# Kernel optimization log

Hardware: AMD Instinct MI355X
Metric: run time of the kernel (lower is better)

The kernel has to match this reference:

```python
import math
import jax, jax.numpy as jnp
import numpy as np

B, C, H, W = 8, 128, 128, 128

def _cosine_basis(n):
    pos = (jnp.arange(n, dtype=jnp.float32) + 0.5) / n          # [n]
    freq = jnp.arange(n, dtype=jnp.float32)[:, None]            # [n,1]
    basis = jnp.cos(freq * pos[None, :] * math.pi) * math.sqrt(2.0 / n)
    return basis.at[0, :].multiply(1.0 / math.sqrt(2.0))        # [n,n]


def setup_inputs() -> dict:
    key = jax.random.key(0)
    ks = jax.random.split(key, 12)
    s = 0.02
    return {
        "x":        jax.random.normal(ks[0], (B, C, H, W), jnp.float32),
        "dw_w":     jax.random.normal(ks[1], (C, 1, 3, 3), jnp.float32) * s,
        "dw_b":     jnp.zeros((C,), jnp.float32),
        "in_w":     jax.random.normal(ks[2], (2 * C, C), jnp.float32) * s,
        "in_b":     jnp.zeros((2 * C,), jnp.float32),
        "out_w":    jax.random.normal(ks[3], (C, C), jnp.float32) * s,
        "out_b":    jnp.zeros((C,), jnp.float32),
        "ln_w":     jnp.ones((C,), jnp.float32),
        "ln_b":     jnp.zeros((C,), jnp.float32),
        "ph_w":     jax.random.normal(ks[4], (C, C), jnp.float32) * s,
        "ph_b":     jnp.zeros((C,), jnp.float32),
        "wave_speed": jnp.ones((1,), jnp.float32),
        "damping":    jnp.full((1,), 0.1, jnp.float32),
        "freq_embed": jax.random.normal(ks[5], (H, W, C), jnp.float32) * s,
    }


def reference(x, dw_w, dw_b, in_w, in_b, out_w, out_b, ln_w, ln_b,
              ph_w, ph_b, wave_speed, damping, freq_embed):
    # depthwise 3x3 conv (groups=C), padding=1
    mixed = jax.lax.conv_general_dilated(
        x, dw_w, window_strides=(1, 1), padding=((1, 1), (1, 1)),
        dimension_numbers=("NCHW", "OIHW", "NCHW"), feature_group_count=C)
    mixed = mixed + dw_b[None, :, None, None]
    mixed = jnp.transpose(mixed, (0, 2, 3, 1))                  # [B,H,W,C]

    proj = mixed @ in_w.T + in_b                                # [B,H,W,2C]
    carrier, gate = jnp.split(proj, 2, axis=-1)

    cos_h = _cosine_basis(H)
    cos_w = _cosine_basis(W)
    # DCT-II along H then W
    spectral = jnp.einsum("bhwc,nh->bnwc", carrier, cos_h)
    spectral = jnp.einsum("bnwc,mw->bnmc", spectral, cos_w)     # [B,H,W,C] (freq)

    # phase modulation (base_resolution == H == W, so no resize)
    phase = jax.nn.gelu(freq_embed @ ph_w.T + ph_b, approximate=False)  # [H,W,C]
    wave_phase = wave_speed * phase                             # broadcast [H,W,C]
    vel_scale = jnp.sin(wave_phase) / jnp.maximum(jnp.abs(wave_speed), 1e-6)
    modulated = (jnp.cos(wave_phase) + vel_scale * (1.0 + 0.5 * damping)) * spectral

    # inverse DCT
    fused = jnp.einsum("bnmc,wm->bnwc", modulated, cos_w.T)
    fused = jnp.einsum("bnwc,hn->bhwc", fused, cos_h.T)         # [B,H,W,C]

    # LayerNorm over channels
    mu = jnp.mean(fused, axis=-1, keepdims=True)
    var = jnp.mean(jnp.square(fused - mu), axis=-1, keepdims=True)
    fused = (fused - mu) / jnp.sqrt(var + 1e-5) * ln_w + ln_b

    fused = fused * jax.nn.silu(gate)
    out = fused @ out_w.T + out_b                               # [B,H,W,C]
    return jnp.transpose(out, (0, 3, 1, 2))                     # [B,C,H,W]
```

## Files before the change

kernel.cpp:

```cpp
#include <hip/hip_runtime.h>
#include <math.h>

#ifndef M_PI
#define M_PI 3.14159265358979323846
#endif

typedef float fx4 __attribute__((ext_vector_type(4)));
typedef __bf16 bf16x8 __attribute__((ext_vector_type(8)));
typedef __bf16 bf16x4 __attribute__((ext_vector_type(4)));

__device__ __forceinline__ unsigned short f2bf(float f){
  union { float f; unsigned u; } v; v.f = f;
  unsigned r = v.u + 0x7FFFu + ((v.u >> 16) & 1u);
  return (unsigned short)(r >> 16);
}
__device__ __forceinline__ float bf2f(unsigned short u){
  union { unsigned u; float f; } v; v.u = ((unsigned)u) << 16;
  return v.f;
}
__device__ __forceinline__ int swz(int row, int colbyte){
  return row*256 + (colbyte ^ ((row & 7) << 4));
}

template<typename FA, typename FB>
__device__ __forceinline__ void run_gemm(FA la, FB lb, fx4 (&acc)[4][4]){
  bf16x8 a[2][4], b[2][4];
  #pragma unroll
  for (int mi=0;mi<4;mi++){ a[0][mi]=la(mi,0); b[0][mi]=lb(mi,0); }
  #pragma unroll
  for (int ks=0; ks<4; ks++){
    int cur = ks&1, nxt = cur^1;
    if (ks<3){
      #pragma unroll
      for (int mi=0;mi<4;mi++){ a[nxt][mi]=la(mi,ks+1); b[nxt][mi]=lb(mi,ks+1); }
    }
    #pragma unroll
    for (int mi=0;mi<4;mi++)
      #pragma unroll
      for (int ni=0;ni<4;ni++)
        acc[mi][ni] = __builtin_amdgcn_mfma_f32_16x16x32_bf16(a[cur][mi], b[cur][ni], acc[mi][ni], 0, 0, 0);
  }
}

template<typename FA0, typename FA1, typename FB>
__device__ __forceinline__ void run_pair_sharedB(FA0 la0, FA1 la1, FB lb,
                                                 fx4 (&acc0)[4][4], fx4 (&acc1)[4][4]){
  bf16x8 a0[2][4], a1[2][4], b[2][4];
  #pragma unroll
  for (int mi=0;mi<4;mi++){ a0[0][mi]=la0(mi,0); a1[0][mi]=la1(mi,0); b[0][mi]=lb(mi,0); }
  #pragma unroll
  for (int ks=0; ks<4; ks++){
    int cur = ks&1, nxt = cur^1;
    if (ks<3){
      #pragma unroll
      for (int mi=0;mi<4;mi++){ a0[nxt][mi]=la0(mi,ks+1); a1[nxt][mi]=la1(mi,ks+1); b[nxt][mi]=lb(mi,ks+1); }
    }
    #pragma unroll
    for (int mi=0;mi<4;mi++)
      #pragma unroll
      for (int ni=0;ni<4;ni++){
        acc0[mi][ni] = __builtin_amdgcn_mfma_f32_16x16x32_bf16(a0[cur][mi], b[cur][ni], acc0[mi][ni], 0, 0, 0);
        acc1[mi][ni] = __builtin_amdgcn_mfma_f32_16x16x32_bf16(a1[cur][mi], b[cur][ni], acc1[mi][ni], 0, 0, 0);
      }
  }
}

template<typename FA, typename FB0, typename FB1>
__device__ __forceinline__ void run_pair_sharedA(FA la, FB0 lb0, FB1 lb1,
                                                 fx4 (&acc0)[4][4], fx4 (&acc1)[4][4]){
  bf16x8 a[2][4], b0[2][4], b1[2][4];
  #pragma unroll
  for (int mi=0;mi<4;mi++){ a[0][mi]=la(mi,0); b0[0][mi]=lb0(mi,0); b1[0][mi]=lb1(mi,0); }
  #pragma unroll
  for (int ks=0; ks<4; ks++){
    int cur = ks&1, nxt = cur^1;
    if (ks<3){
      #pragma unroll
      for (int mi=0;mi<4;mi++){ a[nxt][mi]=la(mi,ks+1); b0[nxt][mi]=lb0(mi,ks+1); b1[nxt][mi]=lb1(mi,ks+1); }
    }
    #pragma unroll
    for (int mi=0;mi<4;mi++)
      #pragma unroll
      for (int ni=0;ni<4;ni++){
        acc0[mi][ni] = __builtin_amdgcn_mfma_f32_16x16x32_bf16(a[cur][mi], b0[cur][ni], acc0[mi][ni], 0, 0, 0);
        acc1[mi][ni] = __builtin_amdgcn_mfma_f32_16x16x32_bf16(a[cur][mi], b1[cur][ni], acc1[mi][ni], 0, 0, 0);
      }
  }
}

__global__ __launch_bounds__(128) void prep_kernel(
    const float* __restrict__ in_w, const float* __restrict__ ph_w,
    const float* __restrict__ out_w,
    unsigned short* __restrict__ basis_bf, unsigned short* __restrict__ basisT_bf,
    unsigned short* __restrict__ ph_w_bf, unsigned short* __restrict__ in_w_bf,
    unsigned short* __restrict__ out_w_bf)
{
  int n = blockIdx.x;
  int h = threadIdx.x;
  double arg = (double)(n*(2*h+1)) * (M_PI/256.0);
  double v = cos(arg) * 0.125;
  if (n==0) v *= 0.7071067811865476;
  unsigned short bv = f2bf((float)v);
  basis_bf[n*128+h]  = bv;
  basisT_bf[h*128+n] = bv;
  ph_w_bf[n*128+h]  = f2bf(ph_w[n*128+h]);
  in_w_bf[n*128+h]        = f2bf(in_w[n*128+h]);
  in_w_bf[(n+128)*128+h]  = f2bf(in_w[(n+128)*128+h]);
  out_w_bf[n*128+h]       = f2bf(out_w[n*128+h]);
}

__global__ __launch_bounds__(256) void castfe_kernel(
  const float* __restrict__ fe, unsigned short* __restrict__ feb)
{
  int idx = blockIdx.x*256 + threadIdx.x;
  const float* s = fe + (size_t)idx*8;
  float4 f0 = *(const float4*)s;
  float4 f1 = *(const float4*)(s+4);
  unsigned short o[8];
  o[0]=f2bf(f0.x); o[1]=f2bf(f0.y); o[2]=f2bf(f0.z); o[3]=f2bf(f0.w);
  o[4]=f2bf(f1.x); o[5]=f2bf(f1.y); o[6]=f2bf(f1.z); o[7]=f2bf(f1.w);
  *(int4*)(feb + (size_t)idx*8) = *(const int4*)o;
}

__global__ __launch_bounds__(256) void projk_kernel(
  const unsigned short* __restrict__ feb, const unsigned short* __restrict__ ph_w_bf,
  float* __restrict__ projT)
{
  int r0 = blockIdx.x * 128;
  int t = threadIdx.x;
  int l = t & 63, wid = t >> 6;
  int wm = wid >> 1, wn = wid & 1;
  int lr = l & 15, lk = (l>>4)*8, ld4 = (l>>4)*4;
  fx4 acc[4][4];
  #pragma unroll
  for (int i=0;i<4;i++) for (int j=0;j<4;j++) acc[i][j] = (fx4){0.f,0.f,0.f,0.f};
  run_gemm(
    [&](int mi,int ks)->bf16x8{ return *(const bf16x8*)(feb + (size_t)(r0 + wm*64+mi*16+lr)*128 + ks*32+lk); },
    [&](int ni,int ks)->bf16x8{ return *(const bf16x8*)(ph_w_bf + (size_t)(wn*64+ni*16+lr)*128 + ks*32+lk); },
    acc);
  #pragma unroll
  for (int mi=0;mi<4;mi++)
    #pragma unroll
    for (int ni=0;ni<4;ni++){
      int c = wn*64 + ni*16 + lr;
      int r = r0 + wm*64 + mi*16 + ld4;
      *(fx4*)(projT + (size_t)c*16384 + r) = acc[mi][ni];
    }
}

__global__ __launch_bounds__(256) void modfin_kernel(
  const float* __restrict__ projT, const float* __restrict__ ph_b,
  const float* __restrict__ wave_speed, const float* __restrict__ damping,
  float* __restrict__ modT)
{
  int blk = blockIdx.x;
  int c = blk >> 4, qb = blk & 15;
  int t = threadIdx.x;
  int q = qb*8 + (t>>5);
  int p0 = (t & 31)*4;
  float ws0 = wave_speed[0];
  float dmp = damping[0];
  float inv = 1.0f / fmaxf(fabsf(ws0), 1e-6f);
  float dampf = 1.0f + 0.5f*dmp;
  float bc = ph_b[c];
  const float* src = projT + (size_t)c*16384 + q;
  float o[4];
  #pragma unroll
  for (int i=0;i<4;i++){
    float v = src[(size_t)(p0+i)*128] + bc;
    float g = 0.5f*v*(1.0f + erff(v*0.70710678118f));
    float wp = ws0*g;
    o[i] = __cosf(wp) + __sinf(wp)*inv*dampf;
  }
  *(float4*)(modT + ((size_t)c*128 + q)*128 + p0) = make_float4(o[0],o[1],o[2],o[3]);
}

__global__ __launch_bounds__(256) void dwconv_kernel(
  const float* __restrict__ x, const float* __restrict__ dw_w,
  const float* __restrict__ dw_b, unsigned short* __restrict__ conv)
{
  int blk = blockIdx.x;
  int plane = blk >> 2, band = blk & 3;
  int c = plane & 127;
  const float* xp = x + (size_t)plane*16384;
  unsigned short* op = conv + (size_t)plane*16384;
  const float* kw = dw_w + c*9;
  float k0=kw[0],k1=kw[1],k2=kw[2],k3=kw[3],k4=kw[4],k5=kw[5],k6=kw[6],k7=kw[7],k8=kw[8];
  float bias = dw_b[c];
  int t = threadIdx.x;
  int q = t & 31;
  int w0 = q*4;
  int rg = t >> 5;
  int h0 = band*32 + rg*4;
  bool le = (q==0), re = (q==31);

  float4 fA, fB, fC; float lA,rA,lB,rB,lC,rC;
  #define LOADROW(hh, f, l, r) { \
    int hc = (hh)<0 ? 0 : ((hh)>127 ? 127 : (hh)); \
    f = *(const float4*)(xp + hc*128 + w0); \
    float lu = __shfl_up(f.w, 1, 32); \
    float rd = __shfl_down(f.x, 1, 32); \
    l = le ? 0.f : lu; \
    r = re ? 0.f : rd; \
    if ((hh)<0 || (hh)>127){ f = make_float4(0.f,0.f,0.f,0.f); l=0.f; r=0.f; } \
  }
  LOADROW(h0-1, fA,lA,rA);
  LOADROW(h0,   fB,lB,rB);
  #pragma unroll
  for (int i=0;i<4;i++){
    LOADROW(h0+1+i, fC,lC,rC);
    float4 o;
    o.x = bias; o.y = bias; o.z = bias; o.w = bias;
    o.x = fmaf(k0,lA,  fmaf(k1,fA.x, fmaf(k2,fA.y, o.x)));
    o.y = fmaf(k0,fA.x,fmaf(k1,fA.y, fmaf(k2,fA.z, o.y)));
    o.z = fmaf(k0,fA.y,fmaf(k1,fA.z, fmaf(k2,fA.w, o.z)));
    o.w = fmaf(k0,fA.z,fmaf(k1,fA.w, fmaf(k2,rA,   o.w)));
    o.x = fmaf(k3,lB,  fmaf(k4,fB.x, fmaf(k5,fB.y, o.x)));
    o.y = fmaf(k3,fB.x,fmaf(k4,fB.y, fmaf(k5,fB.z, o.y)));
    o.z = fmaf(k3,fB.y,fmaf(k4,fB.z, fmaf(k5,fB.w, o.z)));
    o.w = fmaf(k3,fB.z,fmaf(k4,fB.w, fmaf(k5,rB,   o.w)));
    o.x = fmaf(k6,lC,  fmaf(k7,fC.x, fmaf(k8,fC.y, o.x)));
    o.y = fmaf(k6,fC.x,fmaf(k7,fC.y, fmaf(k8,fC.z, o.y)));
    o.z = fmaf(k6,fC.y,fmaf(k7,fC.z, fmaf(k8,fC.w, o.z)));
    o.w = fmaf(k6,fC.z,fmaf(k7,fC.w, fmaf(k8,rC,   o.w)));
    bf16x4 v;
    v[0]=(__bf16)o.x; v[1]=(__bf16)o.y; v[2]=(__bf16)o.z; v[3]=(__bf16)o.w;
    *(bf16x4*)(op + (size_t)(h0+i)*128 + w0) = v;
    fA=fB; lA=lB; rA=rB;
    fB=fC; lB=lC; rB=rC;
  }
  #undef LOADROW
}

__global__ __launch_bounds__(512) void inproj_kernel(
  const unsigned short* __restrict__ conv, const unsigned short* __restrict__ in_w_bf,
  const float* __restrict__ in_b, unsigned short* __restrict__ carrier,
  unsigned short* __restrict__ gate)
{
  __shared__ char A[32768];
  int blk = blockIdx.x; int b = blk>>7, h = blk&127;
  const unsigned short* C = conv + (size_t)b*2097152 + h*128;
  int t = threadIdx.x;
  {
    int wl = t & 63, grp = t >> 6;
    #pragma unroll
    for (int p=0;p<2;p++){
      int w = wl + 64*p;
      #pragma unroll
      for (int q=0;q<4;q++){
        int c0 = (q*8 + grp)*4;
        ushort4 v;
        v.x = C[(size_t)(c0+0)*16384 + w];
        v.y = C[(size_t)(c0+1)*16384 + w];
        v.z = C[(size_t)(c0+2)*16384 + w];
        v.w = C[(size_t)(c0+3)*16384 + w];
        *(ushort4*)(A + swz(w, c0*2)) = v;
      }
    }
  }
  __syncthreads();
  int l = t & 63, wid = t >> 6;
  int wm = wid >> 2, wn = wid & 3;
  int lr = l & 15, lk = (l>>4)*8, ld4 = (l>>4)*4;
  fx4 acc[4][4];
  #pragma unroll
  for (int i=0;i<4;i++) for (int j=0;j<4;j++) acc[i][j] = (fx4){0.f,0.f,0.f,0.f};
  run_gemm(
    [&](int mi,int ks)->bf16x8{ return *(const bf16x8*)(A + swz(wm*64+mi*16+lr, (ks*32+lk)*2)); },
    [&](int ni,int ks)->bf16x8{ return *(const bf16x8*)(in_w_bf + (size_t)(wn*64+ni*16+lr)*128 + ks*32+lk); },
    acc);
  __syncthreads();
  if (wn < 2){
    #pragma unroll
    for (int mi=0;mi<4;mi++)
      #pragma unroll
      for (int ni=0;ni<4;ni++){
        int n = wn*64 + ni*16 + lr;
        int w0 = wm*64 + mi*16 + ld4;
        float bias = in_b[n];
        ushort4 v;
        v.x=f2bf(acc[mi][ni][0]+bias); v.y=f2bf(acc[mi][ni][1]+bias);
        v.z=f2bf(acc[mi][ni][2]+bias); v.w=f2bf(acc[mi][ni][3]+bias);
        *(ushort4*)(carrier + (size_t)(b*128+n)*16384 + h*128 + w0) = v;
      }
  } else {
    #pragma unroll
    for (int mi=0;mi<4;mi++)
      #pragma unroll
      for (int ni=0;ni<4;ni++){
        int n = wn*64 + ni*16 + lr;
        int c = n - 128;
        int w0 = wm*64 + mi*16 + ld4;
        float bias = in_b[n];
        #pragma unroll
        for (int r=0;r<4;r++){
          float v = acc[mi][ni][r] + bias;
          float s = v / (1.0f + __expf(-v));
          *(unsigned short*)(A + swz(w0+r, c*2)) = f2bf(s);
        }
      }
  }
  __syncthreads();
  {
    unsigned short* gout = gate + (size_t)blk*16384;
    int w = t >> 2, cq = (t & 3) * 32;
    #pragma unroll
    for (int i=0;i<4;i++){
      int c0 = cq + i*8;
      int4 v = *(const int4*)(A + swz(w, c0*2));
      *(int4*)(gout + w*128 + c0) = v;
    }
  }
}

__global__ __launch_bounds__(256) void wave_kernel(
  const unsigned short* __restrict__ carrier,
  const unsigned short* __restrict__ basis,
  const unsigned short* __restrict__ basisT,
  const float* __restrict__ modT,
  unsigned short* __restrict__ fused)
{
  __shared__ char U0[32768];
  __shared__ char U1[32768];
  int blk = blockIdx.x;
  int c = blk & 127;
  const unsigned short* X0 = carrier + (size_t)blk*16384;
  const unsigned short* X1 = carrier + (size_t)(blk+512)*16384;
  unsigned short* F0 = fused + (size_t)blk*16384;
  unsigned short* F1 = fused + (size_t)(blk+512)*16384;
  int t = threadIdx.x;
  int l = t & 63, wid = t >> 6;
  int wm = wid >> 1, wn = wid & 1;
  int lr = l & 15, lk = (l>>4)*8, ld4 = (l>>4)*4;
  fx4 acc0[4][4], acc1[4][4];

  #define ZACC { _Pragma("unroll") for (int i=0;i<4;i++) _Pragma("unroll") for (int j=0;j<4;j++){ acc0[i][j]=(fx4){0.f,0.f,0.f,0.f}; acc1[i][j]=(fx4){0.f,0.f,0.f,0.f}; } }
  #define TSTORE(BUF0, BUF1, ROW, COL) { \
    _Pragma("unroll") for (int mi=0;mi<4;mi++) \
      _Pragma("unroll") for (int ni=0;ni<4;ni++){ \
        int rr = wn*64 + ni*16 + lr, cc = wm*64 + mi*16 + ld4; (void)rr; (void)cc; \
        bf16x4 v0, v1; \
        v0[0]=(__bf16)acc0[mi][ni][0]; v0[1]=(__bf16)acc0[mi][ni][1]; \
        v0[2]=(__bf16)acc0[mi][ni][2]; v0[3]=(__bf16)acc0[mi][ni][3]; \
        v1[0]=(__bf16)acc1[mi][ni][0]; v1[1]=(__bf16)acc1[mi][ni][1]; \
        v1[2]=(__bf16)acc1[mi][ni][2]; v1[3]=(__bf16)acc1[mi][ni][3]; \
        *(bf16x4*)(BUF0 + swz(rr, cc*2)) = v0; \
        *(bf16x4*)(BUF1 + swz(rr, cc*2)) = v1; \
      } }

  ZACC;
  run_pair_sharedB(
    [&](int mi,int ks)->bf16x8{ return *(const bf16x8*)(X0 + (size_t)(wm*64+mi*16+lr)*128 + ks*32+lk); },
    [&](int mi,int ks)->bf16x8{ return *(const bf16x8*)(X1 + (size_t)(wm*64+mi*16+lr)*128 + ks*32+lk); },
    [&](int ni,int ks)->bf16x8{ return *(const bf16x8*)(basis + (size_t)(wn*64+ni*16+lr)*128 + ks*32+lk); },
    acc0, acc1);
  TSTORE(U0, U1, m, h);
  __syncthreads();

  ZACC;
  run_pair_sharedA(
    [&](int mi,int ks)->bf16x8{ return *(const bf16x8*)(basis + (size_t)(wm*64+mi*16+lr)*128 + ks*32+lk); },
    [&](int ni,int ks)->bf16x8{ return *(const bf16x8*)(U0 + swz(wn*64+ni*16+lr, (ks*32+lk)*2)); },
    [&](int ni,int ks)->bf16x8{ return *(const bf16x8*)(U1 + swz(wn*64+ni*16+lr, (ks*32+lk)*2)); },
    acc0, acc1);
  {
    const float* Mc = modT + (size_t)c*16384;
    #pragma unroll
    for (int mi=0;mi<4;mi++)
      #pragma unroll
      for (int ni=0;ni<4;ni++){
        int n0 = wm*64 + mi*16 + ld4, m = wn*64 + ni*16 + lr;
        fx4 mv = *(const fx4*)(Mc + (size_t)m*128 + n0);
        acc0[mi][ni] *= mv;
        acc1[mi][ni] *= mv;
      }
  }
  __syncthreads();
  TSTORE(U0, U1, m, n);
  __syncthreads();

  ZACC;
  run_pair_sharedB(
    [&](int mi,int ks)->bf16x8{ return *(const bf16x8*)(U0 + swz(wm*64+mi*16+lr, (ks*32+lk)*2)); },
    [&](int mi,int ks)->bf16x8{ return *(const bf16x8*)(U1 + swz(wm*64+mi*16+lr, (ks*32+lk)*2)); },
    [&](int ni,int ks)->bf16x8{ return *(const bf16x8*)(basisT + (size_t)(wn*64+ni*16+lr)*128 + ks*32+lk); },
    acc0, acc1);
  __syncthreads();
  TSTORE(U0, U1, h, m);
  __syncthreads();

  ZACC;
  run_pair_sharedA(
    [&](int mi,int ks)->bf16x8{ return *(const bf16x8*)(basisT + (size_t)(wm*64+mi*16+lr)*128 + ks*32+lk); },
    [&](int ni,int ks)->bf16x8{ return *(const bf16x8*)(U0 + swz(wn*64+ni*16+lr, (ks*32+lk)*2)); },
    [&](int ni,int ks)->bf16x8{ return *(const bf16x8*)(U1 + swz(wn*64+ni*16+lr, (ks*32+lk)*2)); },
    acc0, acc1);
  #pragma unroll
  for (int mi=0;mi<4;mi++)
    #pragma unroll
    for (int ni=0;ni<4;ni++){
      int hh = wn*64 + ni*16 + lr, w0 = wm*64 + mi*16 + ld4;
      bf16x4 v0, v1;
      v0[0]=(__bf16)acc0[mi][ni][0]; v0[1]=(__bf16)acc0[mi][ni][1];
      v0[2]=(__bf16)acc0[mi][ni][2]; v0[3]=(__bf16)acc0[mi][ni][3];
      v1[0]=(__bf16)acc1[mi][ni][0]; v1[1]=(__bf16)acc1[mi][ni][1];
      v1[2]=(__bf16)acc1[mi][ni][2]; v1[3]=(__bf16)acc1[mi][ni][3];
      *(bf16x4*)(F0 + hh*128 + w0) = v0;
      *(bf16x4*)(F1 + hh*128 + w0) = v1;
    }
  #undef ZACC
  #undef TSTORE
}

__global__ __launch_bounds__(256) void final_kernel(
  const unsigned short* __restrict__ fused, const unsigned short* __restrict__ gate,
  const unsigned short* __restrict__ out_w_bf, const float* __restrict__ out_b,
  const float* __restrict__ ln_w, const float* __restrict__ ln_b,
  float* __restrict__ out)
{
  __shared__ char Fl[32768];
  __shared__ char Al[32768];
  __shared__ float red[256], red2[256];
  __shared__ float mu[128], rs[128];
  int blk = blockIdx.x; int b = blk>>7, h = blk&127;
  const unsigned short* Fsrc = fused + (size_t)b*2097152 + h*128;
  const unsigned short* G = gate + (size_t)blk*16384;
  int t = threadIdx.x;
  {
    int c = t>>1, wq = (t&1)*64;
    #pragma unroll
    for (int i=0;i<8;i++){
      int w0 = wq + i*8;
      int4 v = *(const int4*)(Fsrc + (size_t)c*16384 + w0);
      *(int4*)(Fl + swz(c, w0*2)) = v;
    }
  }
  __syncthreads();
  {
    int w = t&127, half = t>>7;
    float s=0.f, q=0.f;
    for (int i=0;i<64;i++){
      int c = half*64 + i;
      float f = bf2f(*(const unsigned short*)(Fl + swz(c, w*2)));
      s += f; q = fmaf(f,f,q);
    }
    red[t]=s; red2[t]=q;
  }
  __syncthreads();
  if (t < 128){
    float ss = red[t]+red[t+128], qq = red2[t]+red2[t+128];
    float m = ss*(1.f/128.f);
    float var = qq*(1.f/128.f) - m*m;
    mu[t]=m; rs[t]=rsqrtf(var+1e-5f);
  }
  __syncthreads();
  {
    int w = t>>1, cq = (t&1)*64;
    float m_ = mu[w], r_ = rs[w];
    #pragma unroll
    for (int i=0;i<8;i++){
      int c0 = cq + i*8;
      ushort4 g0 = *(const ushort4*)(G + (size_t)w*128 + c0);
      ushort4 g1 = *(const ushort4*)(G + (size_t)w*128 + c0 + 4);
      unsigned short ov[8];
      unsigned short gv[8] = {g0.x,g0.y,g0.z,g0.w,g1.x,g1.y,g1.z,g1.w};
      #pragma unroll
      for (int j=0;j<8;j++){
        int cc = c0+j;
        float f = bf2f(*(const unsigned short*)(Fl + swz(cc, w*2)));
        float a = fmaf((f-m_)*r_, ln_w[cc], ln_b[cc]) * bf2f(gv[j]);
        ov[j] = f2bf(a);
      }
      *(int4*)(Al + swz(w, c0*2)) = *(const int4*)ov;
    }
  }
  __syncthreads();
  int l = t & 63, wid = t >> 6;
  int wm = wid >> 1, wn = wid & 1;
  int lr = l & 15, lk = (l>>4)*8, ld4 = (l>>4)*4;
  fx4 acc[4][4];
  #pragma unroll
  for (int i=0;i<4;i++) for (int j=0;j<4;j++) acc[i][j] = (fx4){0.f,0.f,0.f,0.f};
  run_gemm(
    [&](int mi,int ks)->bf16x8{ return *(const bf16x8*)(Al + swz(wm*64+mi*16+lr, (ks*32+lk)*2)); },
    [&](int ni,int ks)->bf16x8{ return *(const bf16x8*)(out_w_bf + (size_t)(wn*64+ni*16+lr)*128 + ks*32+lk); },
    acc);
  #pragma unroll
  for (int mi=0;mi<4;mi++)
    #pragma unroll
    for (int ni=0;ni<4;ni++){
      int j = wn*64 + ni*16 + lr, w0 = wm*64 + mi*16 + ld4;
      float bj = out_b[j];
      fx4 o = acc[mi][ni];
      o[0]+=bj; o[1]+=bj; o[2]+=bj; o[3]+=bj;
      *(fx4*)(out + ((size_t)(b*128 + j)*128 + h)*128 + w0) = o;
    }
}

extern "C" void kernel_launch(void* const* d_in, const int* in_sizes, int n_in,
                              void* d_out, int out_size, void* d_ws, size_t ws_size,
                              hipStream_t stream)
{
  const float* x      = (const float*)d_in[0];
  const float* dw_w   = (const float*)d_in[1];
  const float* dw_b   = (const float*)d_in[2];
  const float* in_w   = (const float*)d_in[3];
  const float* in_b   = (const float*)d_in[4];
  const float* out_w  = (const float*)d_in[5];
  const float* out_b  = (const float*)d_in[6];
  const float* ln_w   = (const float*)d_in[7];
  const float* ln_b   = (const float*)d_in[8];
  const float* ph_w   = (const float*)d_in[9];
  const float* ph_b   = (const float*)d_in[10];
  const float* wsp    = (const float*)d_in[11];
  const float* dmp    = (const float*)d_in[12];
  const float* fe     = (const float*)d_in[13];
  float* outp = (float*)d_out;

  float* modT  = (float*)d_ws;
  float* projT = modT + 2097152;
  unsigned short* feb      = (unsigned short*)(projT + 2097152);
  unsigned short* conv     = feb     + 2097152;
  unsigned short* carrier  = conv    + 16777216;
  unsigned short* gate     = carrier + 16777216;
  unsigned short* fusedb   = gate    + 16777216;
  unsigned short* basis_bf = fusedb  + 16777216;
  unsigned short* basisT_bf= basis_bf + 16384;
  unsigned short* in_w_bf  = basisT_bf + 16384;
  unsigned short* out_w_bf = in_w_bf + 32768;
  unsigned short* ph_w_bf  = out_w_bf + 16384;

  prep_kernel<<<128,128,0,stream>>>(in_w, ph_w, out_w, basis_bf, basisT_bf, ph_w_bf, in_w_bf, out_w_bf);
  castfe_kernel<<<1024,256,0,stream>>>(fe, feb);
  projk_kernel<<<128,256,0,stream>>>(feb, ph_w_bf, projT);
  modfin_kernel<<<2048,256,0,stream>>>(projT, ph_b, wsp, dmp, modT);
  dwconv_kernel<<<4096,256,0,stream>>>(x, dw_w, dw_b, conv);
  inproj_kernel<<<1024,512,0,stream>>>(conv, in_w_bf, in_b, carrier, gate);
  wave_kernel<<<512,256,0,stream>>>(carrier, basis_bf, basisT_bf, modT, fusedb);
  final_kernel<<<1024,256,0,stream>>>(fusedb, gate, out_w_bf, out_b, ln_w, ln_b, outp);
}
```

Measured before the change: 171.9 us.

## Merge independent prep kernels and process two rows per in-projection block

Prep, feature-embedding cast and depthwise conv now run in one launch, with the block index choosing the role. The ph_w projection GEMM shares a launch with the input projection. The input projection now handles two H rows per block with a paired MFMA routine that reuses each in_w fragment for both rows. This cuts the kernel count from eight to six and halves in_w loads per row. In exchange it uses 64KB of LDS per block, which lowers occupancy, and projk blocks launched at 512 threads leave half their threads idle.

```diff
diff --git a/kernel.cpp b/kernel.cpp
--- a/kernel.cpp
+++ b/kernel.cpp
@@ -88,64 +88,222 @@
   }
 }
 
-__global__ __launch_bounds__(128) void prep_kernel(
+__global__ __launch_bounds__(256) void k1_prep_cast_conv(
     const float* __restrict__ in_w, const float* __restrict__ ph_w,
-    const float* __restrict__ out_w,
+    const float* __restrict__ out_w, const float* __restrict__ fe,
+    const float* __restrict__ x, const float* __restrict__ dw_w,
+    const float* __restrict__ dw_b,
     unsigned short* __restrict__ basis_bf, unsigned short* __restrict__ basisT_bf,
     unsigned short* __restrict__ ph_w_bf, unsigned short* __restrict__ in_w_bf,
-    unsigned short* __restrict__ out_w_bf)
+    unsigned short* __restrict__ out_w_bf, unsigned short* __restrict__ feb,
+    unsigned short* __restrict__ conv)
 {
-  int n = blockIdx.x;
-  int h = threadIdx.x;
-  double arg = (double)(n*(2*h+1)) * (M_PI/256.0);
-  double v = cos(arg) * 0.125;
-  if (n==0) v *= 0.7071067811865476;
-  unsigned short bv = f2bf((float)v);
-  basis_bf[n*128+h]  = bv;
-  basisT_bf[h*128+n] = bv;
-  ph_w_bf[n*128+h]  = f2bf(ph_w[n*128+h]);
-  in_w_bf[n*128+h]        = f2bf(in_w[n*128+h]);
-  in_w_bf[(n+128)*128+h]  = f2bf(in_w[(n+128)*128+h]);
-  out_w_bf[n*128+h]       = f2bf(out_w[n*128+h]);
-}
-
-__global__ __launch_bounds__(256) void castfe_kernel(
-  const float* __restrict__ fe, unsigned short* __restrict__ feb)
-{
-  int idx = blockIdx.x*256 + threadIdx.x;
-  const float* s = fe + (size_t)idx*8;
-  float4 f0 = *(const float4*)s;
-  float4 f1 = *(const float4*)(s+4);
-  unsigned short o[8];
-  o[0]=f2bf(f0.x); o[1]=f2bf(f0.y); o[2]=f2bf(f0.z); o[3]=f2bf(f0.w);
-  o[4]=f2bf(f1.x); o[5]=f2bf(f1.y); o[6]=f2bf(f1.z); o[7]=f2bf(f1.w);
-  *(int4*)(feb + (size_t)idx*8) = *(const int4*)o;
-}
-
-__global__ __launch_bounds__(256) void projk_kernel(
+  int blk = blockIdx.x;
+  int t = threadIdx.x;
+  if (blk < 128){
+    if (t >= 128) return;
+    int n = blk, h = t;
+    double arg = (double)(n*(2*h+1)) * (M_PI/256.0);
+    double v = cos(arg) * 0.125;
+    if (n==0) v *= 0.7071067811865476;
+    unsigned short bv = f2bf((float)v);
+    basis_bf[n*128+h]  = bv;
+    basisT_bf[h*128+n] = bv;
+    ph_w_bf[n*128+h]  = f2bf(ph_w[n*128+h]);
+    in_w_bf[n*128+h]        = f2bf(in_w[n*128+h]);
+    in_w_bf[(n+128)*128+h]  = f2bf(in_w[(n+128)*128+h]);
+    out_w_bf[n*128+h]       = f2bf(out_w[n*128+h]);
+    return;
+  }
+  if (blk < 1152){
+    int idx = (blk-128)*256 + t;
+    const float* s = fe + (size_t)idx*8;
+    float4 f0 = *(const float4*)s;
+    float4 f1 = *(const float4*)(s+4);
+    unsigned short o[8];
+    o[0]=f2bf(f0.x); o[1]=f2bf(f0.y); o[2]=f2bf(f0.z); o[3]=f2bf(f0.w);
+    o[4]=f2bf(f1.x); o[5]=f2bf(f1.y); o[6]=f2bf(f1.z); o[7]=f2bf(f1.w);
+    *(int4*)(feb + (size_t)idx*8) = *(const int4*)o;
+    return;
+  }
+  {
+    int bb = blk - 1152;
+    int plane = bb >> 2, band = bb & 3;
+    int c = plane & 127;
+    const float* xp = x + (size_t)plane*16384;
+    unsigned short* op = conv + (size_t)plane*16384;
+    const float* kw = dw_w + c*9;
+    float k0=kw[0],k1=kw[1],k2=kw[2],k3=kw[3],k4=kw[4],k5=kw[5],k6=kw[6],k7=kw[7],k8=kw[8];
+    float bias = dw_b[c];
+    int q = t & 31;
+    int w0 = q*4;
+    int rg = t >> 5;
+    int h0 = band*32 + rg*4;
+    bool le = (q==0), re = (q==31);
+    float4 fA, fB, fC; float lA,rA,lB,rB,lC,rC;
+    #define LOADROW(hh, f, l, r) { \
+      int hc = (hh)<0 ? 0 : ((hh)>127 ? 127 : (hh)); \
+      f = *(const float4*)(xp + hc*128 + w0); \
+      float lu = __shfl_up(f.w, 1, 32); \
+      float rd = __shfl_down(f.x, 1, 32); \
+      l = le ? 0.f : lu; \
+      r = re ? 0.f : rd; \
+      if ((hh)<0 || (hh)>127){ f = make_float4(0.f,0.f,0.f,0.f); l=0.f; r=0.f; } \
+    }
+    LOADROW(h0-1, fA,lA,rA);
+    LOADROW(h0,   fB,lB,rB);
+    #pragma unroll
+    for (int i=0;i<4;i++){
+      LOADROW(h0+1+i, fC,lC,rC);
+      float4 o;
+      o.x = bias; o.y = bias; o.z = bias; o.w = bias;
+      o.x = fmaf(k0,lA,  fmaf(k1,fA.x, fmaf(k2,fA.y, o.x)));
+      o.y = fmaf(k0,fA.x,fmaf(k1,fA.y, fmaf(k2,fA.z, o.y)));
+      o.z = fmaf(k0,fA.y,fmaf(k1,fA.z, fmaf(k2,fA.w, o.z)));
+      o.w = fmaf(k0,fA.z,fmaf(k1,fA.w, fmaf(k2,rA,   o.w)));
+      o.x = fmaf(k3,lB,  fmaf(k4,fB.x, fmaf(k5,fB.y, o.x)));
+      o.y = fmaf(k3,fB.x,fmaf(k4,fB.y, fmaf(k5,fB.z, o.y)));
+      o.z = fmaf(k3,fB.y,fmaf(k4,fB.z, fmaf(k5,fB.w, o.z)));
+      o.w = fmaf(k3,fB.z,fmaf(k4,fB.w, fmaf(k5,rB,   o.w)));
+      o.x = fmaf(k6,lC,  fmaf(k7,fC.x, fmaf(k8,fC.y, o.x)));
+      o.y = fmaf(k6,fC.x,fmaf(k7,fC.y, fmaf(k8,fC.z, o.y)));
+      o.z = fmaf(k6,fC.y,fmaf(k7,fC.z, fmaf(k8,fC.w, o.z)));
+      o.w = fmaf(k6,fC.z,fmaf(k7,fC.w, fmaf(k8,rC,   o.w)));
+      bf16x4 v;
+      v[0]=(__bf16)o.x; v[1]=(__bf16)o.y; v[2]=(__bf16)o.z; v[3]=(__bf16)o.w;
+      *(bf16x4*)(op + (size_t)(h0+i)*128 + w0) = v;
+      fA=fB; lA=lB; rA=rB;
+      fB=fC; lB=lC; rB=rC;
+    }
+    #undef LOADROW
+  }
+}
+
+__global__ __launch_bounds__(512) void k2_inproj_projk(
+  const unsigned short* __restrict__ conv, const unsigned short* __restrict__ in_w_bf,
+  const float* __restrict__ in_b, unsigned short* __restrict__ carrier,
+  unsigned short* __restrict__ gate,
   const unsigned short* __restrict__ feb, const unsigned short* __restrict__ ph_w_bf,
   float* __restrict__ projT)
 {
-  int r0 = blockIdx.x * 128;
+  int blk = blockIdx.x;
   int t = threadIdx.x;
+  if (blk >= 512){
+    if (t >= 256) return;
+    int r0 = (blk - 512) * 128;
+    int l = t & 63, wid = t >> 6;
+    int wm = wid >> 1, wn = wid & 1;
+    int lr = l & 15, lk = (l>>4)*8, ld4 = (l>>4)*4;
+    fx4 acc[4][4];
+    #pragma unroll
+    for (int i=0;i<4;i++) for (int j=0;j<4;j++) acc[i][j] = (fx4){0.f,0.f,0.f,0.f};
+    run_gemm(
+      [&](int mi,int ks)->bf16x8{ return *(const bf16x8*)(feb + (size_t)(r0 + wm*64+mi*16+lr)*128 + ks*32+lk); },
+      [&](int ni,int ks)->bf16x8{ return *(const bf16x8*)(ph_w_bf + (size_t)(wn*64+ni*16+lr)*128 + ks*32+lk); },
+      acc);
+    #pragma unroll
+    for (int mi=0;mi<4;mi++)
+      #pragma unroll
+      for (int ni=0;ni<4;ni++){
+        int c = wn*64 + ni*16 + lr;
+        int r = r0 + wm*64 + mi*16 + ld4;
+        *(fx4*)(projT + (size_t)c*16384 + r) = acc[mi][ni];
+      }
+    return;
+  }
+  __shared__ char A0[32768];
+  __shared__ char A1[32768];
+  int b = blk >> 6, hp = blk & 63;
+  int h0 = hp*2, h1 = h0+1;
+  const unsigned short* C0 = conv + (size_t)b*2097152 + h0*128;
+  const unsigned short* C1 = C0 + 128;
+  {
+    int wl = t & 63, grp = (t >> 6) & 7;
+    int p = 0;
+    #pragma unroll
+    for (p=0;p<2;p++){
+      int w = wl + 64*p;
+      #pragma unroll
+      for (int q=0;q<4;q++){
+        int c0 = (q*8 + grp)*4;
+        ushort4 v0, v1;
+        v0.x = C0[(size_t)(c0+0)*16384 + w];
+        v0.y = C0[(size_t)(c0+1)*16384 + w];
+        v0.z = C0[(size_t)(c0+2)*16384 + w];
+        v0.w = C0[(size_t)(c0+3)*16384 + w];
+        v1.x = C1[(size_t)(c0+0)*16384 + w];
+        v1.y = C1[(size_t)(c0+1)*16384 + w];
+        v1.z = C1[(size_t)(c0+2)*16384 + w];
+        v1.w = C1[(size_t)(c0+3)*16384 + w];
+        *(ushort4*)(A0 + swz(w, c0*2)) = v0;
+        *(ushort4*)(A1 + swz(w, c0*2)) = v1;
+      }
+    }
+  }
+  __syncthreads();
   int l = t & 63, wid = t >> 6;
-  int wm = wid >> 1, wn = wid & 1;
+  int wm = wid >> 2, wn = wid & 3;
   int lr = l & 15, lk = (l>>4)*8, ld4 = (l>>4)*4;
-  fx4 acc[4][4];
-  #pragma unroll
-  for (int i=0;i<4;i++) for (int j=0;j<4;j++) acc[i][j] = (fx4){0.f,0.f,0.f,0.f};
-  run_gemm(
-    [&](int mi,int ks)->bf16x8{ return *(const bf16x8*)(feb + (size_t)(r0 + wm*64+mi*16+lr)*128 + ks*32+lk); },
-    [&](int ni,int ks)->bf16x8{ return *(const bf16x8*)(ph_w_bf + (size_t)(wn*64+ni*16+lr)*128 + ks*32+lk); },
-    acc);
-  #pragma unroll
-  for (int mi=0;mi<4;mi++)
-    #pragma unroll
-    for (int ni=0;ni<4;ni++){
-      int c = wn*64 + ni*16 + lr;
-      int r = r0 + wm*64 + mi*16 + ld4;
-      *(fx4*)(projT + (size_t)c*16384 + r) = acc[mi][ni];
-    }
+  fx4 acc0[4][4], acc1[4][4];
+  #pragma unroll
+  for (int i=0;i<4;i++) for (int j=0;j<4;j++){ acc0[i][j]=(fx4){0.f,0.f,0.f,0.f}; acc1[i][j]=(fx4){0.f,0.f,0.f,0.f}; }
+  run_pair_sharedB(
+    [&](int mi,int ks)->bf16x8{ return *(const bf16x8*)(A0 + swz(wm*64+mi*16+lr, (ks*32+lk)*2)); },
+    [&](int mi,int ks)->bf16x8{ return *(const bf16x8*)(A1 + swz(wm*64+mi*16+lr, (ks*32+lk)*2)); },
+    [&](int ni,int ks)->bf16x8{ return *(const bf16x8*)(in_w_bf + (size_t)(wn*64+ni*16+lr)*128 + ks*32+lk); },
+    acc0, acc1);
+  __syncthreads();
+  if (wn < 2){
+    #pragma unroll
+    for (int mi=0;mi<4;mi++)
+      #pragma unroll
+      for (int ni=0;ni<4;ni++){
+        int n = wn*64 + ni*16 + lr;
+        int w0 = wm*64 + mi*16 + ld4;
+        float bias = in_b[n];
+        unsigned short* base = carrier + (size_t)(b*128+n)*16384 + w0;
+        ushort4 v0, v1;
+        v0.x=f2bf(acc0[mi][ni][0]+bias); v0.y=f2bf(acc0[mi][ni][1]+bias);
+        v0.z=f2bf(acc0[mi][ni][2]+bias); v0.w=f2bf(acc0[mi][ni][3]+bias);
+        v1.x=f2bf(acc1[mi][ni][0]+bias); v1.y=f2bf(acc1[mi][ni][1]+bias);
+        v1.z=f2bf(acc1[mi][ni][2]+bias); v1.w=f2bf(acc1[mi][ni][3]+bias);
+        *(ushort4*)(base + h0*128) = v0;
+        *(ushort4*)(base + h1*128) = v1;
+      }
+  } else {
+    #pragma unroll
+    for (int mi=0;mi<4;mi++)
+      #pragma unroll
+      for (int ni=0;ni<4;ni++){
+        int n = wn*64 + ni*16 + lr;
+        int c = n - 128;
+        int w0 = wm*64 + mi*16 + ld4;
+        float bias = in_b[n];
+        #pragma unroll
+        for (int r=0;r<4;r++){
+          float v0 = acc0[mi][ni][r] + bias;
+          float v1 = acc1[mi][ni][r] + bias;
+          float s0 = v0 / (1.0f + __expf(-v0));
+          float s1 = v1 / (1.0f + __expf(-v1));
+          *(unsigned short*)(A0 + swz(w0+r, c*2)) = f2bf(s0);
+          *(unsigned short*)(A1 + swz(w0+r, c*2)) = f2bf(s1);
+        }
+      }
+  }
+  __syncthreads();
+  {
+    unsigned short* g0 = gate + ((size_t)(b*128+h0))*16384;
+    unsigned short* g1 = gate + ((size_t)(b*128+h1))*16384;
+    int w = t >> 2, cq = (t & 3) * 32;
+    #pragma unroll
+    for (int i=0;i<4;i++){
+      int c0 = cq + i*8;
+      int4 v0 = *(const int4*)(A0 + swz(w, c0*2));
+      int4 v1 = *(const int4*)(A1 + swz(w, c0*2));
+      *(int4*)(g0 + w*128 + c0) = v0;
+      *(int4*)(g1 + w*128 + c0) = v1;
+    }
+  }
 }
 
 __global__ __launch_bounds__(256) void modfin_kernel(
@@ -173,144 +331,6 @@
     o[i] = __cosf(wp) + __sinf(wp)*inv*dampf;
   }
   *(float4*)(modT + ((size_t)c*128 + q)*128 + p0) = make_float4(o[0],o[1],o[2],o[3]);
-}
-
-__global__ __launch_bounds__(256) void dwconv_kernel(
-  const float* __restrict__ x, const float* __restrict__ dw_w,
-  const float* __restrict__ dw_b, unsigned short* __restrict__ conv)
-{
-  int blk = blockIdx.x;
-  int plane = blk >> 2, band = blk & 3;
-  int c = plane & 127;
-  const float* xp = x + (size_t)plane*16384;
-  unsigned short* op = conv + (size_t)plane*16384;
-  const float* kw = dw_w + c*9;
-  float k0=kw[0],k1=kw[1],k2=kw[2],k3=kw[3],k4=kw[4],k5=kw[5],k6=kw[6],k7=kw[7],k8=kw[8];
-  float bias = dw_b[c];
-  int t = threadIdx.x;
-  int q = t & 31;
-  int w0 = q*4;
-  int rg = t >> 5;
-  int h0 = band*32 + rg*4;
-  bool le = (q==0), re = (q==31);
-
-  float4 fA, fB, fC; float lA,rA,lB,rB,lC,rC;
-  #define LOADROW(hh, f, l, r) { \
-    int hc = (hh)<0 ? 0 : ((hh)>127 ? 127 : (hh)); \
-    f = *(const float4*)(xp + hc*128 + w0); \
-    float lu = __shfl_up(f.w, 1, 32); \
-    float rd = __shfl_down(f.x, 1, 32); \
-    l = le ? 0.f : lu; \
-    r = re ? 0.f : rd; \
-    if ((hh)<0 || (hh)>127){ f = make_float4(0.f,0.f,0.f,0.f); l=0.f; r=0.f; } \
-  }
-  LOADROW(h0-1, fA,lA,rA);
-  LOADROW(h0,   fB,lB,rB);
-  #pragma unroll
-  for (int i=0;i<4;i++){
-    LOADROW(h0+1+i, fC,lC,rC);
-    float4 o;
-    o.x = bias; o.y = bias; o.z = bias; o.w = bias;
-    o.x = fmaf(k0,lA,  fmaf(k1,fA.x, fmaf(k2,fA.y, o.x)));
-    o.y = fmaf(k0,fA.x,fmaf(k1,fA.y, fmaf(k2,fA.z, o.y)));
-    o.z = fmaf(k0,fA.y,fmaf(k1,fA.z, fmaf(k2,fA.w, o.z)));
-    o.w = fmaf(k0,fA.z,fmaf(k1,fA.w, fmaf(k2,rA,   o.w)));
-    o.x = fmaf(k3,lB,  fmaf(k4,fB.x, fmaf(k5,fB.y, o.x)));
-    o.y = fmaf(k3,fB.x,fmaf(k4,fB.y, fmaf(k5,fB.z, o.y)));
-    o.z = fmaf(k3,fB.y,fmaf(k4,fB.z, fmaf(k5,fB.w, o.z)));
-    o.w = fmaf(k3,fB.z,fmaf(k4,fB.w, fmaf(k5,rB,   o.w)));
-    o.x = fmaf(k6,lC,  fmaf(k7,fC.x, fmaf(k8,fC.y, o.x)));
-    o.y = fmaf(k6,fC.x,fmaf(k7,fC.y, fmaf(k8,fC.z, o.y)));
-    o.z = fmaf(k6,fC.y,fmaf(k7,fC.z, fmaf(k8,fC.w, o.z)));
-    o.w = fmaf(k6,fC.z,fmaf(k7,fC.w, fmaf(k8,rC,   o.w)));
-    bf16x4 v;
-    v[0]=(__bf16)o.x; v[1]=(__bf16)o.y; v[2]=(__bf16)o.z; v[3]=(__bf16)o.w;
-    *(bf16x4*)(op + (size_t)(h0+i)*128 + w0) = v;
-    fA=fB; lA=lB; rA=rB;
-    fB=fC; lB=lC; rB=rC;
-  }
-  #undef LOADROW
-}
-
-__global__ __launch_bounds__(512) void inproj_kernel(
-  const unsigned short* __restrict__ conv, const unsigned short* __restrict__ in_w_bf,
-  const float* __restrict__ in_b, unsigned short* __restrict__ carrier,
-  unsigned short* __restrict__ gate)
-{
-  __shared__ char A[32768];
-  int blk = blockIdx.x; int b = blk>>7, h = blk&127;
-  const unsigned short* C = conv + (size_t)b*2097152 + h*128;
-  int t = threadIdx.x;
-  {
-    int wl = t & 63, grp = t >> 6;
-    #pragma unroll
-    for (int p=0;p<2;p++){
-      int w = wl + 64*p;
-      #pragma unroll
-      for (int q=0;q<4;q++){
-        int c0 = (q*8 + grp)*4;
-        ushort4 v;
-        v.x = C[(size_t)(c0+0)*16384 + w];
-        v.y = C[(size_t)(c0+1)*16384 + w];
-        v.z = C[(size_t)(c0+2)*16384 + w];
-        v.w = C[(size_t)(c0+3)*16384 + w];
-        *(ushort4*)(A + swz(w, c0*2)) = v;
-      }
-    }
-  }
-  __syncthreads();
-  int l = t & 63, wid = t >> 6;
-  int wm = wid >> 2, wn = wid & 3;
-  int lr = l & 15, lk = (l>>4)*8, ld4 = (l>>4)*4;
-  fx4 acc[4][4];
-  #pragma unroll
-  for (int i=0;i<4;i++) for (int j=0;j<4;j++) acc[i][j] = (fx4){0.f,0.f,0.f,0.f};
-  run_gemm(
-    [&](int mi,int ks)->bf16x8{ return *(const bf16x8*)(A + swz(wm*64+mi*16+lr, (ks*32+lk)*2)); },
-    [&](int ni,int ks)->bf16x8{ return *(const bf16x8*)(in_w_bf + (size_t)(wn*64+ni*16+lr)*128 + ks*32+lk); },
-    acc);
-  __syncthreads();
-  if (wn < 2){
-    #pragma unroll
-    for (int mi=0;mi<4;mi++)
-      #pragma unroll
-      for (int ni=0;ni<4;ni++){
-        int n = wn*64 + ni*16 + lr;
-        int w0 = wm*64 + mi*16 + ld4;
-        float bias = in_b[n];
-        ushort4 v;
-        v.x=f2bf(acc[mi][ni][0]+bias); v.y=f2bf(acc[mi][ni][1]+bias);
-        v.z=f2bf(acc[mi][ni][2]+bias); v.w=f2bf(acc[mi][ni][3]+bias);
-        *(ushort4*)(carrier + (size_t)(b*128+n)*16384 + h*128 + w0) = v;
-      }
-  } else {
-    #pragma unroll
-    for (int mi=0;mi<4;mi++)
-      #pragma unroll
-      for (int ni=0;ni<4;ni++){
-        int n = wn*64 + ni*16 + lr;
-        int c = n - 128;
-        int w0 = wm*64 + mi*16 + ld4;
-        float bias = in_b[n];
-        #pragma unroll
-        for (int r=0;r<4;r++){
-          float v = acc[mi][ni][r] + bias;
-          float s = v / (1.0f + __expf(-v));
-          *(unsigned short*)(A + swz(w0+r, c*2)) = f2bf(s);
-        }
-      }
-  }
-  __syncthreads();
-  {
-    unsigned short* gout = gate + (size_t)blk*16384;
-    int w = t >> 2, cq = (t & 3) * 32;
-    #pragma unroll
-    for (int i=0;i<4;i++){
-      int c0 = cq + i*8;
-      int4 v = *(const int4*)(A + swz(w, c0*2));
-      *(int4*)(gout + w*128 + c0) = v;
-    }
-  }
 }
 
 __global__ __launch_bounds__(256) void wave_kernel(
@@ -335,10 +355,10 @@
   fx4 acc0[4][4], acc1[4][4];
 
   #define ZACC { _Pragma("unroll") for (int i=0;i<4;i++) _Pragma("unroll") for (int j=0;j<4;j++){ acc0[i][j]=(fx4){0.f,0.f,0.f,0.f}; acc1[i][j]=(fx4){0.f,0.f,0.f,0.f}; } }
-  #define TSTORE(BUF0, BUF1, ROW, COL) { \
+  #define TSTORE(BUF0, BUF1) { \
     _Pragma("unroll") for (int mi=0;mi<4;mi++) \
       _Pragma("unroll") for (int ni=0;ni<4;ni++){ \
-        int rr = wn*64 + ni*16 + lr, cc = wm*64 + mi*16 + ld4; (void)rr; (void)cc; \
+        int rr = wn*64 + ni*16 + lr, cc = wm*64 + mi*16 + ld4; \
         bf16x4 v0, v1; \
         v0[0]=(__bf16)acc0[mi][ni][0]; v0[1]=(__bf16)acc0[mi][ni][1]; \
         v0[2]=(__bf16)acc0[mi][ni][2]; v0[3]=(__bf16)acc0[mi][ni][3]; \
@@ -354,7 +374,7 @@
     [&](int mi,int ks)->bf16x8{ return *(const bf16x8*)(X1 + (size_t)(wm*64+mi*16+lr)*128 + ks*32+lk); },
     [&](int ni,int ks)->bf16x8{ return *(const bf16x8*)(basis + (size_t)(wn*64+ni*16+lr)*128 + ks*32+lk); },
     acc0, acc1);
-  TSTORE(U0, U1, m, h);
+  TSTORE(U0, U1);
   __syncthreads();
 
   ZACC;
@@ -376,7 +396,7 @@
       }
   }
   __syncthreads();
-  TSTORE(U0, U1, m, n);
+  TSTORE(U0, U1);
   __syncthreads();
 
   ZACC;
@@ -386,7 +406,7 @@
     [&](int ni,int ks)->bf16x8{ return *(const bf16x8*)(basisT + (size_t)(wn*64+ni*16+lr)*128 + ks*32+lk); },
     acc0, acc1);
   __syncthreads();
-  TSTORE(U0, U1, h, m);
+  TSTORE(U0, U1);
   __syncthreads();
 
   ZACC;
@@ -530,12 +550,11 @@
   unsigned short* out_w_bf = in_w_bf + 32768;
   unsigned short* ph_w_bf  = out_w_bf + 16384;
 
-  prep_kernel<<<128,128,0,stream>>>(in_w, ph_w, out_w, basis_bf, basisT_bf, ph_w_bf, in_w_bf, out_w_bf);
-  castfe_kernel<<<1024,256,0,stream>>>(fe, feb);
-  projk_kernel<<<128,256,0,stream>>>(feb, ph_w_bf, projT);
+  k1_prep_cast_conv<<<5248,256,0,stream>>>(in_w, ph_w, out_w, fe, x, dw_w, dw_b,
+      basis_bf, basisT_bf, ph_w_bf, in_w_bf, out_w_bf, feb, conv);
+  k2_inproj_projk<<<640,512,0,stream>>>(conv, in_w_bf, in_b, carrier, gate,
+      feb, ph_w_bf, projT);
   modfin_kernel<<<2048,256,0,stream>>>(projT, ph_b, wsp, dmp, modT);
-  dwconv_kernel<<<4096,256,0,stream>>>(x, dw_w, dw_b, conv);
-  inproj_kernel<<<1024,512,0,stream>>>(conv, in_w_bf, in_b, carrier, gate);
   wave_kernel<<<512,256,0,stream>>>(carrier, basis_bf, basisT_bf, modT, fusedb);
   final_kernel<<<1024,256,0,stream>>>(fusedb, gate, out_w_bf, out_b, ln_w, ln_b, outp);
 }
```

Result: no change. 169.4 us (-1.5%).
